# Performance work log

Hardware: AMD Instinct MI355X
Metric: run time of the kernel (lower is better)

## Reference

```python
import jax, jax.numpy as jnp
import numpy as np

N_NODES = 256
N_BAGS = 4
BAG_SIZE = 64


def _conv1d(x, w, b):
    # x: [B, C, T], w: [O, I, K], 'same' padding (pad=1, k=3), stride 1
    y = jax.lax.conv_general_dilated(x, w, window_strides=(1,), padding=[(1, 1)],
                                     dimension_numbers=('NCH', 'OIH', 'NCH'))
    return y + b[None, :, None]


def _select_indices(attention, degree):
    # Deterministic analogue of subgraphSelection: top-4 nodes by degree; for each,
    # prob row hrl = (row + row) * 100 (original numpy graph[:][b] is also row b);
    # pick 64 globally-distinct indices (collision avoidance) by probability, sorted.
    _, b4 = jax.lax.top_k(degree, N_BAGS)
    taken = jnp.zeros(N_NODES, dtype=bool)
    rows = []
    for i in range(N_BAGS):  # fixed small loop
        probs = 200.0 * attention[b4[i]]
        masked = jnp.where(taken, -jnp.inf, probs)
        _, idx = jax.lax.top_k(masked, BAG_SIZE)
        idx = jnp.sort(idx)
        taken = taken.at[idx].set(True)
        rows.append(idx)
    return jnp.stack(rows)  # [4, 64] int32


def setup_inputs() -> dict:
    key = jax.random.key(0)
    ks = jax.random.split(key, 13)
    B, T = 32768, N_NODES
    return {
        'attention': jax.random.uniform(ks[0], (N_NODES, N_NODES), jnp.float32),
        'degree': jax.random.uniform(ks[1], (N_NODES,), jnp.float32),
        'x': jax.random.normal(ks[2], (B, T, 1), jnp.float32),
        'conv1_w': jax.random.normal(ks[3], (1, 1, 3), jnp.float32) * 0.01,
        'conv1_b': jnp.zeros((1,), jnp.float32),
        'W1': jax.random.normal(ks[4], (64, 64), jnp.float32) * 0.05,
        'b1': jnp.zeros((64,), jnp.float32),
        'W2': jax.random.normal(ks[5], (64, 64), jnp.float32) * 0.05,
        'b2': jnp.zeros((64,), jnp.float32),
        'Wa': jax.random.normal(ks[6], (64, 64), jnp.float32) * 0.05,
        'ba': jnp.zeros((64,), jnp.float32),
        'conv2_w': jax.random.normal(ks[7], (4, 4, 3), jnp.float32) * 0.01,
        'conv2_b': jnp.zeros((4,), jnp.float32),
    }


def reference(attention, degree, x, conv1_w, conv1_b, W1, b1, W2, b2, Wa, ba, conv2_w, conv2_b):
    idx = _select_indices(attention, degree)            # [4, 64]
    xp = jnp.transpose(x, (0, 2, 1))                    # [B, 1, T]
    # Conv1D_feature_extracter(1,1,3): tanh(dropout(tanh(conv))) -> eval-mode tanh(tanh(conv))
    x_site = jnp.tanh(jnp.tanh(_conv1d(xp, conv1_w, conv1_b)))  # [B, 1, T]
    # mapping_converge: irregular gather x[b, 0, idx] -> [B, 4, 64]
    mx = xp[:, 0, :][:, idx]
    # IMILmask (torch Linear: y = x W^T + b)
    l1 = jax.nn.relu(mx @ W1.T + b1)
    l2 = jax.nn.relu(mx @ W2.T + b2)
    A_imi = jax.nn.sigmoid((l1 + l2) @ Wa.T + ba)
    masked_x = (A_imi + 1.0) * mx                       # [B, 4, 64]
    # Conv1D_feature_extracter(4,4,3)
    x_bag = jnp.tanh(jnp.tanh(_conv1d(masked_x, conv2_w, conv2_b)))  # [B, 4, 64]
    return (x_bag, x_site)
```

## Files before the change

kernel.cpp:

```cpp
#include <hip/hip_runtime.h>
#include <hip/hip_bf16.h>
#include <math.h>


#define NB 16

typedef __bf16 bf16x8 __attribute__((ext_vector_type(8)));
typedef float  f32x4  __attribute__((ext_vector_type(4)));

__device__ __forceinline__ float tanh_poly(float y) {
    float y2 = y * y;
    float p = fmaf(y2, -0.008863829f, 0.021869488f);
    p = fmaf(y2, p, -0.053968254f);
    p = fmaf(y2, p, 0.13333334f);
    p = fmaf(y2, p, -0.33333334f);
    p = fmaf(y2, p, 1.0f);
    return y * p;
}
__device__ __forceinline__ float dtanh2(float y) { return tanh_poly(tanh_poly(y)); }

__device__ __forceinline__ bf16x8 cvt_frag(const float* src) {
    float4 u = *(const float4*)src;
    float4 v = *(const float4*)(src + 4);
    bf16x8 f;
    f[0]=(__bf16)u.x; f[1]=(__bf16)u.y; f[2]=(__bf16)u.z; f[3]=(__bf16)u.w;
    f[4]=(__bf16)v.x; f[5]=(__bf16)v.y; f[6]=(__bf16)v.z; f[7]=(__bf16)v.w;
    return f;
}

__global__ __launch_bounds__(1024) void sel_kernel(
    const float* __restrict__ att, const float* __restrict__ deg,
    const float* __restrict__ W1, const float* __restrict__ W2,
    const float* __restrict__ Wa,
    int* __restrict__ permg)
{
    const int tid = threadIdx.x;

    if (blockIdx.x == 1) {
        bf16x8* w12g = (bf16x8*)(permg + 256);
        bf16x8* w3g  = w12g + 1024;
        {
            int ct = tid >> 7, h = (tid >> 6) & 1, l2 = tid & 63;
            int n = ct * 16 + (l2 & 15);
            int k = h * 32 + (l2 >> 4) * 8;
            const float* src = (n < 64) ? (W1 + n * 64 + k) : (W2 + (n - 64) * 64 + k);
            w12g[ct * 128 + h * 64 + l2] = cvt_frag(src);
        }
        if (tid < 512) {
            int ct = tid >> 7, h = (tid >> 6) & 1, l2 = tid & 63;
            int n = ct * 16 + (l2 & 15);
            int k = h * 32 + (l2 >> 4) * 8;
            w3g[ct * 128 + h * 64 + l2] = cvt_frag(Wa + n * 64 + k);
        }
        return;
    }

    __shared__ __align__(16) float pv[256];
    __shared__ int taken[256];
    __shared__ int part[256][5];
    __shared__ int b4s[4];
    __shared__ unsigned long long wmask[4];

    const int j    = tid & 255;
    const int q    = tid >> 8;
    const int lane = tid & 63;
    const int wv   = tid >> 6;

    if (tid < 256) { taken[tid] = 0; pv[tid] = deg[tid]; }
    __syncthreads();

    for (int rnd = -1; rnd < 4; ++rnd) {
        if (rnd >= 0) {
            if (tid < 256) {
                float p = 200.0f * att[b4s[rnd] * 256 + tid];
                pv[tid] = taken[tid] ? -__builtin_huge_valf() : p;
            }
            __syncthreads();
        }
        {
            float pj = pv[j];
            int cnt = 0;
            const float4* pv4 = (const float4*)&pv[q * 64];
            #pragma unroll
            for (int k4 = 0; k4 < 16; ++k4) {
                float4 v = pv4[k4];
                int kb = q * 64 + k4 * 4;
                cnt += (v.x > pj || (v.x == pj && (kb + 0) < j)) ? 1 : 0;
                cnt += (v.y > pj || (v.y == pj && (kb + 1) < j)) ? 1 : 0;
                cnt += (v.z > pj || (v.z == pj && (kb + 2) < j)) ? 1 : 0;
                cnt += (v.w > pj || (v.w == pj && (kb + 3) < j)) ? 1 : 0;
            }
            part[j][q] = cnt;
        }
        __syncthreads();
        int sel = 0;
        if (tid < 256) {
            int rank = part[tid][0] + part[tid][1] + part[tid][2] + part[tid][3];
            if (rnd < 0) {
                if (rank < 4) b4s[rank] = tid;
            } else {
                sel = (rank < 64) ? 1 : 0;
            }
        }
        if (rnd >= 0) {
            unsigned long long mask = __ballot(sel);
            if (lane == 0 && wv < 4) wmask[wv] = mask;
            __syncthreads();
            if (sel) {
                int pos = __popcll(mask & ((1ull << lane) - 1ull));
                #pragma unroll
                for (int w = 0; w < 4; ++w) if (w < wv) pos += __popcll(wmask[w]);
                permg[rnd * 64 + pos] = tid;
                taken[tid] = 1;
            }
        }
        __syncthreads();
    }
}

__global__ __launch_bounds__(256, 4) void main_kernel(
    const float* __restrict__ x,
    const float* __restrict__ c1w, const float* __restrict__ c1b,
    const float* __restrict__ b1,  const float* __restrict__ b2,
    const float* __restrict__ ba,
    const float* __restrict__ c2w, const float* __restrict__ c2b,
    const int* __restrict__ permg,
    float* __restrict__ out, int Btot)
{
    __shared__ float xls[NB][264];
    __shared__ int perm[256];
    __shared__ __align__(16) unsigned char scratch[4][4352];

    const int tid = threadIdx.x;
    const int batch0 = blockIdx.x * NB;
    const bf16x8* __restrict__ w12g = (const bf16x8*)(permg + 256);
    const bf16x8* __restrict__ w3g  = w12g + 1024;

    #pragma unroll
    for (int i = 0; i < 4; ++i) {
        int flat = i * 1024 + tid * 4;
        int r = flat >> 8, c = flat & 255;
        const float4 v = *(const float4*)&x[(size_t)(batch0 + r) * 256 + c];
        *(float4*)&xls[r][c] = v;
    }
    perm[tid] = permg[tid];
    __syncthreads();

    {
        const float cw0 = c1w[0], cw1 = c1w[1], cw2 = c1w[2], cb = c1b[0];
        const size_t siteBase = (size_t)Btot * 256;
        #pragma unroll
        for (int i = 0; i < 4; ++i) {
            int flat = i * 1024 + tid * 4;
            int r = flat >> 8, c = flat & 255;
            const float* xr = &xls[r][0];
            float xm = (c > 0)       ? xr[c - 1] : 0.0f;
            float x0 = xr[c], x1 = xr[c + 1], x2 = xr[c + 2], x3 = xr[c + 3];
            float xp = (c + 4 < 256) ? xr[c + 4] : 0.0f;
            float4 o4;
            o4.x = dtanh2(fmaf(cw0, xm, fmaf(cw1, x0, fmaf(cw2, x1, cb))));
            o4.y = dtanh2(fmaf(cw0, x0, fmaf(cw1, x1, fmaf(cw2, x2, cb))));
            o4.z = dtanh2(fmaf(cw0, x1, fmaf(cw1, x2, fmaf(cw2, x3, cb))));
            o4.w = dtanh2(fmaf(cw0, x2, fmaf(cw1, x3, fmaf(cw2, xp, cb))));
            *(float4*)&out[siteBase + (size_t)(batch0 + r) * 256 + c] = o4;
        }
    }

    const int l = tid & 63, wvi = tid >> 6;
    const int hi = l >> 4, m = l & 15;

    float b1v[4], b2v[4], bav[4];
    #pragma unroll
    for (int ct = 0; ct < 4; ++ct) {
        b1v[ct] = b1[ct * 16 + m];
        b2v[ct] = b2[ct * 16 + m];
        bav[ct] = ba[ct * 16 + m];
    }

    const int bag = m & 3;
    const int bL  = wvi * 4 + (m >> 2);
    bf16x8 af0, af1;
    #pragma unroll
    for (int jj = 0; jj < 8; ++jj) {
        int k0 = hi * 8 + jj;
        af0[jj] = (__bf16)xls[bL][perm[bag * 64 + k0]];
        af1[jj] = (__bf16)xls[bL][perm[bag * 64 + 32 + k0]];
    }

    f32x4 acc12[8];
    #pragma unroll
    for (int ct = 0; ct < 8; ++ct) acc12[ct] = (f32x4){0.f, 0.f, 0.f, 0.f};
    #pragma unroll
    for (int ct = 0; ct < 8; ++ct) {
        bf16x8 bf0 = w12g[ct * 128 + l];
        bf16x8 bf1 = w12g[ct * 128 + 64 + l];
        acc12[ct] = __builtin_amdgcn_mfma_f32_16x16x32_bf16(af0, bf0, acc12[ct], 0, 0, 0);
        acc12[ct] = __builtin_amdgcn_mfma_f32_16x16x32_bf16(af1, bf1, acc12[ct], 0, 0, 0);
    }

    __bf16* lsb = (__bf16*)scratch[wvi];
    #pragma unroll
    for (int ct = 0; ct < 4; ++ct) {
        #pragma unroll
        for (int qq = 0; qq < 4; ++qq) {
            float a = acc12[ct][qq] + b1v[ct];      a = a > 0.f ? a : 0.f;
            float b = acc12[ct + 4][qq] + b2v[ct];  b = b > 0.f ? b : 0.f;
            lsb[(hi * 4 + qq) * 72 + ct * 16 + m] = (__bf16)(a + b);
        }
    }
    bf16x8 a30 = *(const bf16x8*)(lsb + m * 72 + hi * 8);
    bf16x8 a31 = *(const bf16x8*)(lsb + m * 72 + 32 + hi * 8);

    f32x4 acc3[4];
    #pragma unroll
    for (int ct = 0; ct < 4; ++ct) acc3[ct] = (f32x4){0.f, 0.f, 0.f, 0.f};
    #pragma unroll
    for (int ct = 0; ct < 4; ++ct) {
        bf16x8 bf0 = w3g[ct * 128 + l];
        bf16x8 bf1 = w3g[ct * 128 + 64 + l];
        acc3[ct] = __builtin_amdgcn_mfma_f32_16x16x32_bf16(a30, bf0, acc3[ct], 0, 0, 0);
        acc3[ct] = __builtin_amdgcn_mfma_f32_16x16x32_bf16(a31, bf1, acc3[ct], 0, 0, 0);
    }

    __syncthreads();

    float* msk = (float*)scratch[wvi];
    #pragma unroll
    for (int ct = 0; ct < 4; ++ct) {
        #pragma unroll
        for (int qq = 0; qq < 4; ++qq) {
            float v = acc3[ct][qq] + bav[ct];
            float s = __builtin_amdgcn_rcpf(1.0f + __expf(-v)) + 1.0f;
            int r  = hi * 4 + qq;
            int bq = r >> 2, ii = r & 3;
            int t  = ct * 16 + m;
            float mxv = xls[wvi * 4 + bq][perm[ii * 64 + t]];
            msk[(bq * 4 + ii) * 68 + t] = s * mxv;
        }
    }

    {
        const int bq2 = m >> 2, o = m & 3;
        const int tseg = hi * 16;
        float wv2[4][3];
        #pragma unroll
        for (int ii = 0; ii < 4; ++ii)
            #pragma unroll
            for (int kk = 0; kk < 3; ++kk)
                wv2[ii][kk] = c2w[o * 12 + ii * 3 + kk];
        const float cb2 = c2b[o];

        float mrow[4][16], mm1[4], mp1[4];
        #pragma unroll
        for (int ii = 0; ii < 4; ++ii) {
            const float* base = msk + (bq2 * 4 + ii) * 68;
            #pragma unroll
            for (int ch = 0; ch < 4; ++ch) {
                float4 vv = *(const float4*)(base + tseg + ch * 4);
                mrow[ii][ch * 4 + 0] = vv.x; mrow[ii][ch * 4 + 1] = vv.y;
                mrow[ii][ch * 4 + 2] = vv.z; mrow[ii][ch * 4 + 3] = vv.w;
            }
            mm1[ii] = (tseg > 0)       ? base[tseg - 1]  : 0.0f;
            mp1[ii] = (tseg + 16 < 64) ? base[tseg + 16] : 0.0f;
        }

        float res[16];
        #pragma unroll
        for (int t = 0; t < 16; ++t) {
            float a = cb2;
            #pragma unroll
            for (int ii = 0; ii < 4; ++ii) {
                float xm = (t == 0)  ? mm1[ii] : mrow[ii][t - 1];
                float xc = mrow[ii][t];
                float xp = (t == 15) ? mp1[ii] : mrow[ii][t + 1];
                a = fmaf(wv2[ii][0], xm, a);
                a = fmaf(wv2[ii][1], xc, a);
                a = fmaf(wv2[ii][2], xp, a);
            }
            res[t] = dtanh2(a);
        }
        float* op = out + (size_t)(batch0 + wvi * 4 + bq2) * 256 + o * 64 + tseg;
        #pragma unroll
        for (int ch = 0; ch < 4; ++ch) {
            float4 o4 = { res[ch*4+0], res[ch*4+1], res[ch*4+2], res[ch*4+3] };
            *(float4*)(op + ch * 4) = o4;
        }
    }
}

extern "C" void kernel_launch(void* const* d_in, const int* in_sizes, int n_in,
                              void* d_out, int out_size, void* d_ws, size_t ws_size,
                              hipStream_t stream)
{
    const float* att = (const float*)d_in[0];
    const float* deg = (const float*)d_in[1];
    const float* x   = (const float*)d_in[2];
    const float* c1w = (const float*)d_in[3];
    const float* c1b = (const float*)d_in[4];
    const float* W1  = (const float*)d_in[5];
    const float* b1  = (const float*)d_in[6];
    const float* W2  = (const float*)d_in[7];
    const float* b2  = (const float*)d_in[8];
    const float* Wa  = (const float*)d_in[9];
    const float* ba  = (const float*)d_in[10];
    const float* c2w = (const float*)d_in[11];
    const float* c2b = (const float*)d_in[12];
    float* out = (float*)d_out;
    int* perm  = (int*)d_ws;
    int Btot   = in_sizes[2] / 256;

    hipLaunchKernelGGL(sel_kernel, dim3(2), dim3(1024), 0, stream,
                       att, deg, W1, W2, Wa, perm);
    hipLaunchKernelGGL(main_kernel, dim3(Btot / NB), dim3(256), 0, stream,
                       x, c1w, c1b, b1, b2, ba, c2w, c2b,
                       perm, out, Btot);
}
```

Baseline: 142.5 us.

## Read x directly from global and stage only gathered values per wave in LDS

The block-wide LDS staging of the full x tile and the perm table is removed. Each wave now reads its own four rows straight from global for the site conv, then gathers the permuted elements into a per-wave LDS buffer in bag order, so MFMA A-fragments load as contiguous float4s instead of per-element indirect LDS reads. Block-wide barriers disappear, LDS per block shrinks, and occupancy is raised from 4 to 5 blocks. The cost is extra scattered global reads for the gather and the halo elements, which mostly hit in cache.

```diff
diff --git a/kernel.cpp b/kernel.cpp
--- a/kernel.cpp
+++ b/kernel.cpp
@@ -22,6 +22,12 @@
 __device__ __forceinline__ bf16x8 cvt_frag(const float* src) {
     float4 u = *(const float4*)src;
     float4 v = *(const float4*)(src + 4);
+    bf16x8 f;
+    f[0]=(__bf16)u.x; f[1]=(__bf16)u.y; f[2]=(__bf16)u.z; f[3]=(__bf16)u.w;
+    f[4]=(__bf16)v.x; f[5]=(__bf16)v.y; f[6]=(__bf16)v.z; f[7]=(__bf16)v.w;
+    return f;
+}
+__device__ __forceinline__ bf16x8 pack_bf16x8(float4 u, float4 v) {
     bf16x8 f;
     f[0]=(__bf16)u.x; f[1]=(__bf16)u.y; f[2]=(__bf16)u.z; f[3]=(__bf16)u.w;
     f[4]=(__bf16)v.x; f[5]=(__bf16)v.y; f[6]=(__bf16)v.z; f[7]=(__bf16)v.w;
@@ -118,7 +124,7 @@
     }
 }
 
-__global__ __launch_bounds__(256, 4) void main_kernel(
+__global__ __launch_bounds__(256, 5) void main_kernel(
     const float* __restrict__ x,
     const float* __restrict__ c1w, const float* __restrict__ c1b,
     const float* __restrict__ b1,  const float* __restrict__ b2,
@@ -127,46 +133,46 @@
     const int* __restrict__ permg,
     float* __restrict__ out, int Btot)
 {
-    __shared__ float xls[NB][264];
-    __shared__ int perm[256];
-    __shared__ __align__(16) unsigned char scratch[4][4352];
+    __shared__ float xp[NB][256];
+    __shared__ __align__(16) unsigned char scratch[4][4096];
 
     const int tid = threadIdx.x;
+    const int l   = tid & 63, wvi = tid >> 6;
     const int batch0 = blockIdx.x * NB;
+    const int rowb   = batch0 + wvi * 4;
     const bf16x8* __restrict__ w12g = (const bf16x8*)(permg + 256);
     const bf16x8* __restrict__ w3g  = w12g + 1024;
-
-    #pragma unroll
-    for (int i = 0; i < 4; ++i) {
-        int flat = i * 1024 + tid * 4;
-        int r = flat >> 8, c = flat & 255;
-        const float4 v = *(const float4*)&x[(size_t)(batch0 + r) * 256 + c];
-        *(float4*)&xls[r][c] = v;
-    }
-    perm[tid] = permg[tid];
-    __syncthreads();
 
     {
         const float cw0 = c1w[0], cw1 = c1w[1], cw2 = c1w[2], cb = c1b[0];
         const size_t siteBase = (size_t)Btot * 256;
+        const int c = l * 4;
         #pragma unroll
         for (int i = 0; i < 4; ++i) {
-            int flat = i * 1024 + tid * 4;
-            int r = flat >> 8, c = flat & 255;
-            const float* xr = &xls[r][0];
-            float xm = (c > 0)       ? xr[c - 1] : 0.0f;
-            float x0 = xr[c], x1 = xr[c + 1], x2 = xr[c + 2], x3 = xr[c + 3];
-            float xp = (c + 4 < 256) ? xr[c + 4] : 0.0f;
+            const float* xr = x + (size_t)(rowb + i) * 256;
+            float4 xc = *(const float4*)(xr + c);
+            float xm = (c > 0)   ? xr[c - 1] : 0.0f;
+            float xq = (c < 252) ? xr[c + 4] : 0.0f;
             float4 o4;
-            o4.x = dtanh2(fmaf(cw0, xm, fmaf(cw1, x0, fmaf(cw2, x1, cb))));
-            o4.y = dtanh2(fmaf(cw0, x0, fmaf(cw1, x1, fmaf(cw2, x2, cb))));
-            o4.z = dtanh2(fmaf(cw0, x1, fmaf(cw1, x2, fmaf(cw2, x3, cb))));
-            o4.w = dtanh2(fmaf(cw0, x2, fmaf(cw1, x3, fmaf(cw2, xp, cb))));
-            *(float4*)&out[siteBase + (size_t)(batch0 + r) * 256 + c] = o4;
-        }
-    }
-
-    const int l = tid & 63, wvi = tid >> 6;
+            o4.x = dtanh2(fmaf(cw0, xm,   fmaf(cw1, xc.x, fmaf(cw2, xc.y, cb))));
+            o4.y = dtanh2(fmaf(cw0, xc.x, fmaf(cw1, xc.y, fmaf(cw2, xc.z, cb))));
+            o4.z = dtanh2(fmaf(cw0, xc.y, fmaf(cw1, xc.z, fmaf(cw2, xc.w, cb))));
+            o4.w = dtanh2(fmaf(cw0, xc.z, fmaf(cw1, xc.w, fmaf(cw2, xq,   cb))));
+            *(float4*)&out[siteBase + (size_t)(rowb + i) * 256 + c] = o4;
+        }
+    }
+
+    {
+        const int4 pidx = *(const int4*)(permg + l * 4);
+        #pragma unroll
+        for (int i = 0; i < 4; ++i) {
+            const float* xr = x + (size_t)(rowb + i) * 256;
+            float4 g;
+            g.x = xr[pidx.x]; g.y = xr[pidx.y]; g.z = xr[pidx.z]; g.w = xr[pidx.w];
+            *(float4*)&xp[wvi * 4 + i][l * 4] = g;
+        }
+    }
+
     const int hi = l >> 4, m = l & 15;
 
     float b1v[4], b2v[4], bav[4];
@@ -180,11 +186,10 @@
     const int bag = m & 3;
     const int bL  = wvi * 4 + (m >> 2);
     bf16x8 af0, af1;
-    #pragma unroll
-    for (int jj = 0; jj < 8; ++jj) {
-        int k0 = hi * 8 + jj;
-        af0[jj] = (__bf16)xls[bL][perm[bag * 64 + k0]];
-        af1[jj] = (__bf16)xls[bL][perm[bag * 64 + 32 + k0]];
+    {
+        const float* src = &xp[bL][bag * 64 + hi * 8];
+        af0 = pack_bf16x8(*(const float4*)src,        *(const float4*)(src + 4));
+        af1 = pack_bf16x8(*(const float4*)(src + 32), *(const float4*)(src + 36));
     }
 
     f32x4 acc12[8];
@@ -222,8 +227,6 @@
         acc3[ct] = __builtin_amdgcn_mfma_f32_16x16x32_bf16(a31, bf1, acc3[ct], 0, 0, 0);
     }
 
-    __syncthreads();
-
     float* msk = (float*)scratch[wvi];
     #pragma unroll
     for (int ct = 0; ct < 4; ++ct) {
@@ -231,11 +234,9 @@
         for (int qq = 0; qq < 4; ++qq) {
             float v = acc3[ct][qq] + bav[ct];
             float s = __builtin_amdgcn_rcpf(1.0f + __expf(-v)) + 1.0f;
-            int r  = hi * 4 + qq;
-            int bq = r >> 2, ii = r & 3;
-            int t  = ct * 16 + m;
-            float mxv = xls[wvi * 4 + bq][perm[ii * 64 + t]];
-            msk[(bq * 4 + ii) * 68 + t] = s * mxv;
+            int t = ct * 16 + m;
+            float mxv = xp[wvi * 4 + hi][qq * 64 + t];
+            msk[(hi * 4 + qq) * 64 + t] = s * mxv;
         }
     }
 
@@ -253,7 +254,7 @@
         float mrow[4][16], mm1[4], mp1[4];
         #pragma unroll
         for (int ii = 0; ii < 4; ++ii) {
-            const float* base = msk + (bq2 * 4 + ii) * 68;
+            const float* base = msk + (bq2 * 4 + ii) * 64;
             #pragma unroll
             for (int ch = 0; ch < 4; ++ch) {
                 float4 vv = *(const float4*)(base + tseg + ch * 4);
@@ -270,16 +271,16 @@
             float a = cb2;
             #pragma unroll
             for (int ii = 0; ii < 4; ++ii) {
-                float xm = (t == 0)  ? mm1[ii] : mrow[ii][t - 1];
-                float xc = mrow[ii][t];
-                float xp = (t == 15) ? mp1[ii] : mrow[ii][t + 1];
-                a = fmaf(wv2[ii][0], xm, a);
-                a = fmaf(wv2[ii][1], xc, a);
-                a = fmaf(wv2[ii][2], xp, a);
+                float xm2 = (t == 0)  ? mm1[ii] : mrow[ii][t - 1];
+                float xc2 = mrow[ii][t];
+                float xp2 = (t == 15) ? mp1[ii] : mrow[ii][t + 1];
+                a = fmaf(wv2[ii][0], xm2, a);
+                a = fmaf(wv2[ii][1], xc2, a);
+                a = fmaf(wv2[ii][2], xp2, a);
             }
             res[t] = dtanh2(a);
         }
-        float* op = out + (size_t)(batch0 + wvi * 4 + bq2) * 256 + o * 64 + tseg;
+        float* op = out + (size_t)(rowb + bq2) * 256 + o * 64 + tseg;
         #pragma unroll
         for (int ch = 0; ch < 4; ++ch) {
             float4 o4 = { res[ch*4+0], res[ch*4+1], res[ch*4+2], res[ch*4+3] };
```

Result: slower. 152.9 us (+7.3%).
